# Performance work log

Hardware: AMD Instinct MI355X
Metric: run time of the kernel (lower is better)

Reference implementation:

```python
import jax, jax.numpy as jnp
import numpy as np

HIDDEN = 128
HEADS = 8
HEAD_DIM = HIDDEN // HEADS
N_NODES = 100000
N_EDGES = 1600000


def setup_inputs() -> dict:
    key = jax.random.key(0)
    ks = jax.random.split(key, 12)
    s = 1.0 / np.sqrt(HIDDEN)
    inp = {
        "x": jax.random.normal(ks[0], (N_NODES, HIDDEN), dtype=jnp.float32),
        "edge_index": jax.random.randint(ks[1], (2, N_EDGES), 0, N_NODES, dtype=jnp.int32),
        "edge_emb": jax.random.normal(ks[2], (N_EDGES, HIDDEN), dtype=jnp.float32),
        "q_w": jax.random.uniform(ks[3], (HIDDEN, HIDDEN), jnp.float32, -s, s),
        "q_b": jax.random.uniform(ks[4], (HIDDEN,), jnp.float32, -s, s),
        "k_w": jax.random.uniform(ks[5], (HIDDEN, HIDDEN), jnp.float32, -s, s),
        "k_b": jax.random.uniform(ks[6], (HIDDEN,), jnp.float32, -s, s),
        "v_w": jax.random.uniform(ks[7], (HIDDEN, HIDDEN), jnp.float32, -s, s),
        "v_b": jax.random.uniform(ks[8], (HIDDEN,), jnp.float32, -s, s),
        "out_w": jax.random.uniform(ks[9], (HIDDEN, HIDDEN), jnp.float32, -s, s),
        "out_b": jax.random.uniform(ks[10], (HIDDEN,), jnp.float32, -s, s),
        "eb_w": jax.random.uniform(ks[11], (HEADS, HIDDEN), jnp.float32, -s, s),
        "eb_b": jnp.zeros((HEADS,), dtype=jnp.float32),
    }
    return inp


def reference(x, edge_index, edge_emb, q_w, q_b, k_w, k_b, v_w, v_b, out_w, out_b, eb_w, eb_b):
    n = x.shape[0]
    # node projections -> [N, H, D]
    q = (x @ q_w.T + q_b).reshape(n, HEADS, HEAD_DIM)
    k = (x @ k_w.T + k_b).reshape(n, HEADS, HEAD_DIM)
    v = (x @ v_w.T + v_b).reshape(n, HEADS, HEAD_DIM)

    row, col = edge_index[0], edge_index[1]
    # per-edge scores: [E, H]
    scores = jnp.einsum('ehd,ehd->eh', q[row], k[col]) / jnp.sqrt(jnp.float32(HEAD_DIM))
    scores = scores + edge_emb @ eb_w.T + eb_b

    # segmented softmax over incoming edges of each destination node `row`
    seg_max = jax.ops.segment_max(scores, row, num_segments=n)  # [N, H]
    exp_scores = jnp.exp(scores - seg_max[row])
    seg_sum = jax.ops.segment_sum(exp_scores, row, num_segments=n)  # [N, H]
    attn = exp_scores / (seg_sum[row] + 1e-10)  # [E, H]

    # weighted scatter-aggregation of values
    weighted_v = attn[..., None] * v[col]  # [E, H, D]
    out = jax.ops.segment_sum(weighted_v, row, num_segments=n)  # [N, H, D]
    out = out.reshape(n, HIDDEN)
    return out @ out_w.T + out_b
```

## Files before the change

kernel.cpp:

```cpp
#include <hip/hip_runtime.h>

#define HID 128
#define NH 8

typedef __attribute__((ext_vector_type(8))) short short8;
typedef __attribute__((ext_vector_type(4))) float f32x4;
typedef __attribute__((ext_vector_type(2))) float f32x2;

__device__ __forceinline__ unsigned short f2bf(float f) {
    unsigned int u = __float_as_uint(f);
    u = (u + 0x7FFF + ((u >> 16) & 1)) >> 16;
    return (unsigned short)u;
}
__device__ __forceinline__ float bf2f(unsigned short s) {
    return __uint_as_float((unsigned int)s << 16);
}
__device__ __forceinline__ unsigned int pack2bf(float lo, float hi) {
    return (unsigned int)f2bf(lo) | ((unsigned int)f2bf(hi) << 16);
}

__global__ void k_init(const float* __restrict__ qw, const float* __restrict__ kw,
                       const float* __restrict__ vw, const float* __restrict__ ow,
                       unsigned short* __restrict__ wbf,
                       const int* __restrict__ row, int E, int* __restrict__ count) {
    int bid = blockIdx.x;
    int t = threadIdx.x;
    if (bid < 64) {
        int i = bid * 256 + t;
        int idx = i * 4;
        int m = idx >> 14;
        int off = idx & 16383;
        const float* src = (m == 0) ? qw : (m == 1) ? kw : (m == 2) ? vw : ow;
        float4 v = *(const float4*)(src + off);
        ushort4 o;
        o.x = f2bf(v.x); o.y = f2bf(v.y); o.z = f2bf(v.z); o.w = f2bf(v.w);
        *(ushort4*)(wbf + idx) = o;
    } else {
        int i = (bid - 64) * 256 + t;
        int stride = (gridDim.x - 64) * 256;
        for (; i < E; i += stride) atomicAdd(&count[row[i]], 1);
    }
}

__global__ void k_scan1(const int* __restrict__ in, int total,
                        int* __restrict__ out, int* __restrict__ bsums) {
    __shared__ int sd[256];
    int t = threadIdx.x;
    int base = blockIdx.x * 1024 + t * 4;
    int v0 = (base + 0 < total) ? in[base + 0] : 0;
    int v1 = (base + 1 < total) ? in[base + 1] : 0;
    int v2 = (base + 2 < total) ? in[base + 2] : 0;
    int v3 = (base + 3 < total) ? in[base + 3] : 0;
    int s = v0 + v1 + v2 + v3;
    sd[t] = s; __syncthreads();
    for (int off = 1; off < 256; off <<= 1) {
        int xx = (t >= off) ? sd[t - off] : 0;
        __syncthreads();
        sd[t] += xx;
        __syncthreads();
    }
    int excl = sd[t] - s;
    if (t == 255) bsums[blockIdx.x] = sd[255];
    int run = excl;
    if (base + 0 < total) out[base + 0] = run; run += v0;
    if (base + 1 < total) out[base + 1] = run; run += v1;
    if (base + 2 < total) out[base + 2] = run; run += v2;
    if (base + 3 < total) out[base + 3] = run;
}

__global__ void k_scan2(int* __restrict__ bs, int nb) {
    __shared__ int sd[128];
    int t = threadIdx.x;
    int vv = (t < nb) ? bs[t] : 0;
    sd[t] = vv; __syncthreads();
    for (int off = 1; off < 128; off <<= 1) {
        int xx = (t >= off) ? sd[t - off] : 0;
        __syncthreads();
        sd[t] += xx;
        __syncthreads();
    }
    if (t < nb) bs[t] = sd[t] - vv;
}

__global__ void k_scan3(int* __restrict__ out, int total, const int* __restrict__ bs) {
    int add = bs[blockIdx.x];
    int base = blockIdx.x * 1024 + threadIdx.x * 4;
    #pragma unroll
    for (int i = 0; i < 4; ++i)
        if (base + i < total) out[base + i] += add;
}

__global__ __launch_bounds__(256) void k_fat(
    const float* __restrict__ x, const unsigned short* __restrict__ wbf,
    const float* __restrict__ qb_, const float* __restrict__ kb_, const float* __restrict__ vb_,
    unsigned short* __restrict__ qkvbf, int n, int qblocks,
    const int* __restrict__ row, const int* __restrict__ col,
    const float* __restrict__ emb, const float* __restrict__ ebw,
    const float* __restrict__ ebb, const int* __restrict__ start,
    int* __restrict__ cursor, int* __restrict__ col_sorted,
    unsigned short* __restrict__ bias_s, int E)
{
    __shared__ __align__(16) char sm[17408];
    int bid = blockIdx.x;
    int t = threadIdx.x;

    if (bid < qblocks) {
        unsigned short (*xs)[136] = (unsigned short (*)[136])sm;
        int m0 = bid * 64;
        #pragma unroll
        for (int p = 0; p < 2; ++p) {
            int f = p * 256 + t;
            int r = f >> 3;
            int c16 = (f & 7) * 16;
            int node = m0 + r;
            float4 u0 = {0,0,0,0}, u1 = {0,0,0,0}, u2 = {0,0,0,0}, u3 = {0,0,0,0};
            if (node < n) {
                const float4* px = (const float4*)(x + (size_t)node * HID + c16);
                u0 = px[0]; u1 = px[1]; u2 = px[2]; u3 = px[3];
            }
            union { unsigned short u[8]; short8 v; } a, b;
            a.u[0]=f2bf(u0.x); a.u[1]=f2bf(u0.y); a.u[2]=f2bf(u0.z); a.u[3]=f2bf(u0.w);
            a.u[4]=f2bf(u1.x); a.u[5]=f2bf(u1.y); a.u[6]=f2bf(u1.z); a.u[7]=f2bf(u1.w);
            b.u[0]=f2bf(u2.x); b.u[1]=f2bf(u2.y); b.u[2]=f2bf(u2.z); b.u[3]=f2bf(u2.w);
            b.u[4]=f2bf(u3.x); b.u[5]=f2bf(u3.y); b.u[6]=f2bf(u3.z); b.u[7]=f2bf(u3.w);
            *(short8*)&xs[r][c16]     = a.v;
            *(short8*)&xs[r][c16 + 8] = b.v;
        }
        __syncthreads();

        int w = t >> 6, l = t & 63;
        int lr = l & 15, lc = l >> 4;
        short8 afr[4];
        #pragma unroll
        for (int c = 0; c < 4; ++c)
            afr[c] = *(const short8*)&xs[w * 16 + lr][c * 32 + lc * 8];

        #pragma unroll
        for (int m = 0; m < 3; ++m) {
            const float* bias = (m == 0) ? qb_ : (m == 1) ? kb_ : vb_;
            #pragma unroll
            for (int ct = 0; ct < 8; ++ct) {
                int colg = ct * 16 + lr;
                f32x4 acc = {0.f, 0.f, 0.f, 0.f};
                const unsigned short* wrow = wbf + (size_t)m * 16384 + (size_t)colg * 128 + lc * 8;
                #pragma unroll
                for (int c = 0; c < 4; ++c) {
                    short8 bfr = *(const short8*)(wrow + c * 32);
                    acc = __builtin_amdgcn_mfma_f32_16x16x32_bf16(afr[c], bfr, acc, 0, 0, 0);
                }
                float bv = bias[colg];
                #pragma unroll
                for (int r = 0; r < 4; ++r) {
                    int node = m0 + w * 16 + lc * 4 + r;
                    if (node < n)
                        qkvbf[(size_t)node * 384 + m * 128 + colg] = f2bf(acc[r] + bv);
                }
            }
        }
    } else {
        float (*Wx)[4][8][4] = (float (*)[4][8][4])sm;
        for (int i = t; i < 1024; i += 256) {
            int j = i & 3, g = (i >> 2) & 7, c = (i >> 5) & 3, h = i >> 7;
            Wx[h][c][g][j] = ebw[h * 128 + g * 16 + c * 4 + j];
        }
        float bbr[8];
        #pragma unroll
        for (int i = 0; i < 8; ++i) bbr[i] = ebb[i];
        __syncthreads();

        int l = t & 63;
        int g = l & 7;
        int sub = l >> 3;
        int e = (bid - qblocks) * 32 + (t >> 6) * 8 + sub;
        bool act = e < E;

        float p[8] = {0.f,0.f,0.f,0.f,0.f,0.f,0.f,0.f};
        if (act) {
            const float4* pe = (const float4*)(emb + (size_t)e * HID + g * 16);
            #pragma unroll
            for (int c = 0; c < 4; ++c) {
                float4 ev = pe[c];
                #pragma unroll
                for (int h = 0; h < 8; ++h) {
                    float4 wv = *(const float4*)&Wx[h][c][g][0];
                    p[h] += ev.x*wv.x + ev.y*wv.y + ev.z*wv.z + ev.w*wv.w;
                }
            }
        }
        #pragma unroll
        for (int off = 1; off < 8; off <<= 1) {
            #pragma unroll
            for (int h = 0; h < 8; ++h) p[h] += __shfl_xor(p[h], off);
        }
        if (act && g == 0) {
            int r = row[e];
            int ps = start[r] + atomicAdd(&cursor[r], 1);
            col_sorted[ps] = col[e];
            uint4 bv;
            bv.x = pack2bf(p[0] + bbr[0], p[1] + bbr[1]);
            bv.y = pack2bf(p[2] + bbr[2], p[3] + bbr[3]);
            bv.z = pack2bf(p[4] + bbr[4], p[5] + bbr[5]);
            bv.w = pack2bf(p[6] + bbr[6], p[7] + bbr[7]);
            *(uint4*)(bias_s + (size_t)ps * 8) = bv;
        }
    }
}

__global__ __launch_bounds__(256) void k_cvtk(
    const unsigned short* __restrict__ qkvbf, unsigned char* __restrict__ kp8, int n)
{
    int i = blockIdx.x * 256 + threadIdx.x;
    int node = i >> 4;
    int c8 = (i & 15) * 8;
    if (node >= n) return;
    short8 kv = *(const short8*)(qkvbf + (size_t)node * 384 + 128 + c8);
    float f[8];
    #pragma unroll
    for (int j = 0; j < 8; ++j) f[j] = bf2f((unsigned short)kv[j]);
    unsigned int lo = 0, hi = 0;
    lo = (unsigned int)__builtin_amdgcn_cvt_pk_fp8_f32(f[0], f[1], (int)lo, false);
    lo = (unsigned int)__builtin_amdgcn_cvt_pk_fp8_f32(f[2], f[3], (int)lo, true);
    hi = (unsigned int)__builtin_amdgcn_cvt_pk_fp8_f32(f[4], f[5], (int)hi, false);
    hi = (unsigned int)__builtin_amdgcn_cvt_pk_fp8_f32(f[6], f[7], (int)hi, true);
    uint2 o; o.x = lo; o.y = hi;
    *(uint2*)(kp8 + (size_t)node * HID + c8) = o;
}

__global__ __launch_bounds__(256) void k_attn(
    const unsigned short* __restrict__ qkvbf, const unsigned char* __restrict__ kp8,
    const int* __restrict__ cols, const unsigned short* __restrict__ bias_s,
    const int* __restrict__ start, unsigned short* __restrict__ aout, int n)
{
    int node = blockIdx.x * 4 + (threadIdx.x >> 6);
    if (node >= n) return;
    int l = threadIdx.x & 63;
    int slot = l >> 3;
    int h = l & 7;
    int s0 = start[node];
    int deg = start[node + 1] - s0;

    float qf[16];
    {
        const unsigned short* qp = qkvbf + (size_t)node * 384 + h * 16;
        short8 q0 = *(const short8*)qp;
        short8 q1 = *(const short8*)(qp + 8);
        #pragma unroll
        for (int i = 0; i < 8; ++i) {
            qf[i] = bf2f((unsigned short)q0[i]);
            qf[8 + i] = bf2f((unsigned short)q1[i]);
        }
    }

    float acc[16];
    #pragma unroll
    for (int i = 0; i < 16; ++i) acc[i] = 0.f;
    float denom = 0.f;

    for (int base = 0; base < deg; base += 8) {
        int idx = base + slot;
        bool act = idx < deg;
        int sidx = s0 + (act ? idx : 0);
        int c = act ? cols[sidx] : 0;
        float eb = act ? bf2f(bias_s[(size_t)sidx * 8 + h]) : 0.f;
        uint4 kw4 = *(const uint4*)(kp8 + (size_t)c * HID + h * 16);
        const unsigned short* vp = qkvbf + (size_t)c * 384 + 256 + h * 16;
        short8 va = *(const short8*)vp;
        short8 vb = *(const short8*)(vp + 8);

        float part = 0.f;
        {
            f32x2 d0 = __builtin_amdgcn_cvt_pk_f32_fp8((int)kw4.x, false);
            f32x2 d1 = __builtin_amdgcn_cvt_pk_f32_fp8((int)kw4.x, true);
            f32x2 d2 = __builtin_amdgcn_cvt_pk_f32_fp8((int)kw4.y, false);
            f32x2 d3 = __builtin_amdgcn_cvt_pk_f32_fp8((int)kw4.y, true);
            f32x2 d4 = __builtin_amdgcn_cvt_pk_f32_fp8((int)kw4.z, false);
            f32x2 d5 = __builtin_amdgcn_cvt_pk_f32_fp8((int)kw4.z, true);
            f32x2 d6 = __builtin_amdgcn_cvt_pk_f32_fp8((int)kw4.w, false);
            f32x2 d7 = __builtin_amdgcn_cvt_pk_f32_fp8((int)kw4.w, true);
            part += qf[0]*d0[0] + qf[1]*d0[1] + qf[2]*d1[0] + qf[3]*d1[1];
            part += qf[4]*d2[0] + qf[5]*d2[1] + qf[6]*d3[0] + qf[7]*d3[1];
            part += qf[8]*d4[0] + qf[9]*d4[1] + qf[10]*d5[0] + qf[11]*d5[1];
            part += qf[12]*d6[0] + qf[13]*d6[1] + qf[14]*d7[0] + qf[15]*d7[1];
        }
        float es = act ? __expf(part * 0.25f + eb) : 0.f;
        denom += es;
        #pragma unroll
        for (int i = 0; i < 8; ++i) acc[i]     += es * bf2f((unsigned short)va[i]);
        #pragma unroll
        for (int i = 0; i < 8; ++i) acc[8 + i] += es * bf2f((unsigned short)vb[i]);
    }

    #pragma unroll
    for (int off = 8; off < 64; off <<= 1) {
        denom += __shfl_xor(denom, off);
        #pragma unroll
        for (int i = 0; i < 16; ++i) acc[i] += __shfl_xor(acc[i], off);
    }
    if (slot == 0) {
        float inv = 1.f / (denom + 1e-10f);
        uint4 o0, o1;
        o0.x = pack2bf(acc[0]*inv,  acc[1]*inv);
        o0.y = pack2bf(acc[2]*inv,  acc[3]*inv);
        o0.z = pack2bf(acc[4]*inv,  acc[5]*inv);
        o0.w = pack2bf(acc[6]*inv,  acc[7]*inv);
        o1.x = pack2bf(acc[8]*inv,  acc[9]*inv);
        o1.y = pack2bf(acc[10]*inv, acc[11]*inv);
        o1.z = pack2bf(acc[12]*inv, acc[13]*inv);
        o1.w = pack2bf(acc[14]*inv, acc[15]*inv);
        unsigned short* op = aout + (size_t)node * HID + h * 16;
        *(uint4*)op       = o0;
        *(uint4*)(op + 8) = o1;
    }
}

__global__ __launch_bounds__(256) void k_outproj_mfma(
    const unsigned short* __restrict__ aout, const unsigned short* __restrict__ wbf,
    const float* __restrict__ ob, float* __restrict__ out, int n)
{
    __shared__ unsigned short hs[64][136];
    int t = threadIdx.x;
    int m0 = blockIdx.x * 64;
    #pragma unroll
    for (int p = 0; p < 4; ++p) {
        int f = p * 256 + t;
        int r = f >> 4;
        int c8 = (f & 15) * 8;
        int node = m0 + r;
        short8 val = {0,0,0,0,0,0,0,0};
        if (node < n) val = *(const short8*)(aout + (size_t)node * HID + c8);
        *(short8*)&hs[r][c8] = val;
    }
    __syncthreads();

    int w = t >> 6, l = t & 63;
    int lr = l & 15, lc = l >> 4;
    short8 afr[4];
    #pragma unroll
    for (int c = 0; c < 4; ++c)
        afr[c] = *(const short8*)&hs[w * 16 + lr][c * 32 + lc * 8];

    #pragma unroll
    for (int ct = 0; ct < 8; ++ct) {
        int colg = ct * 16 + lr;
        f32x4 acc = {0.f, 0.f, 0.f, 0.f};
        const unsigned short* wrow = wbf + (size_t)3 * 16384 + (size_t)colg * 128 + lc * 8;
        #pragma unroll
        for (int c = 0; c < 4; ++c) {
            short8 bfr = *(const short8*)(wrow + c * 32);
            acc = __builtin_amdgcn_mfma_f32_16x16x32_bf16(afr[c], bfr, acc, 0, 0, 0);
        }
        float bv = ob[colg];
        #pragma unroll
        for (int r = 0; r < 4; ++r) {
            int node = m0 + w * 16 + lc * 4 + r;
            if (node < n)
                out[(size_t)node * HID + colg] = acc[r] + bv;
        }
    }
}

extern "C" void kernel_launch(void* const* d_in, const int* in_sizes, int n_in,
                              void* d_out, int out_size, void* d_ws, size_t ws_size,
                              hipStream_t stream) {
    const float* x   = (const float*)d_in[0];
    const int*   eix = (const int*)  d_in[1];
    const float* emb = (const float*)d_in[2];
    const float* qw  = (const float*)d_in[3];
    const float* qb  = (const float*)d_in[4];
    const float* kw  = (const float*)d_in[5];
    const float* kb  = (const float*)d_in[6];
    const float* vw  = (const float*)d_in[7];
    const float* vb  = (const float*)d_in[8];
    const float* ow  = (const float*)d_in[9];
    const float* ob  = (const float*)d_in[10];
    const float* ebw = (const float*)d_in[11];
    const float* ebb = (const float*)d_in[12];

    int n = in_sizes[0] / HID;
    int E = in_sizes[2] / HID;
    const int* row = eix;
    const int* col = eix + E;

    char* wsp = (char*)d_ws;
    auto alloc = [&](size_t bytes) -> void* {
        void* p = (void*)wsp;
        wsp += (bytes + 255) & ~(size_t)255;
        return p;
    };
    unsigned short* qkvbf = (unsigned short*)alloc((size_t)n * 384 * 2);
    unsigned char* kp8    = (unsigned char*)alloc((size_t)n * HID);
    unsigned short* wbf   = (unsigned short*)alloc((size_t)4 * 16384 * 2);
    int* col_sorted       = (int*)alloc((size_t)E * 4);
    unsigned short* bias_s= (unsigned short*)alloc((size_t)E * 8 * 2);
    unsigned short* aout  = (unsigned short*)alloc((size_t)n * HID * 2);
    int* count            = (int*)alloc((size_t)(n + 2) * 4);
    int* startp           = (int*)alloc((size_t)(n + 2) * 4);
    int* bsums            = (int*)alloc(256 * 4);
    int* cursor           = (int*)alloc((size_t)n * 4);

    hipMemsetAsync(count, 0, (size_t)(n + 1) * sizeof(int), stream);
    hipMemsetAsync(cursor, 0, (size_t)n * sizeof(int), stream);

    k_init<<<64 + 2048, 256, 0, stream>>>(qw, kw, vw, ow, wbf, row, E, count);

    int total = n + 1;
    int nb = (total + 1023) / 1024;
    k_scan1<<<nb, 256, 0, stream>>>(count, total, startp, bsums);
    k_scan2<<<1, 128, 0, stream>>>(bsums, nb);
    k_scan3<<<nb, 256, 0, stream>>>(startp, total, bsums);

    int qblocks = (n + 63) / 64;
    int eblocks = (E + 31) / 32;
    k_fat<<<qblocks + eblocks, 256, 0, stream>>>(
        x, wbf, qb, kb, vb, qkvbf, n, qblocks,
        row, col, emb, ebw, ebb, startp, cursor, col_sorted, bias_s, E);

    k_cvtk<<<(n * 16 + 255) / 256, 256, 0, stream>>>(qkvbf, kp8, n);

    k_attn<<<(n + 3) / 4, 256, 0, stream>>>(qkvbf, kp8, col_sorted, bias_s,
                                            startp, aout, n);
    k_outproj_mfma<<<(n + 63) / 64, 256, 0, stream>>>(aout, wbf, ob, (float*)d_out, n);
}
```

Before: 557.2 us.

## Fold scan fixup into consumers, merge memsets, add L2 prewarm pass

Removes the k_scan3 fixup kernel: k_fat and k_attn now add the per-block prefix from bsums when they read start offsets. The two memsets become one by placing count and cursor next to each other in the workspace. It also adds a prewarm kernel that streams the qkv and fp8 key buffers just before attention so they sit in cache for the gathers. The prewarm costs a full extra read of about 100MB, and the scan change adds one extra load per lookup.

```diff
diff --git a/kernel.cpp b/kernel.cpp
--- a/kernel.cpp
+++ b/kernel.cpp
@@ -82,13 +82,6 @@
     if (t < nb) bs[t] = sd[t] - vv;
 }
 
-__global__ void k_scan3(int* __restrict__ out, int total, const int* __restrict__ bs) {
-    int add = bs[blockIdx.x];
-    int base = blockIdx.x * 1024 + threadIdx.x * 4;
-    #pragma unroll
-    for (int i = 0; i < 4; ++i)
-        if (base + i < total) out[base + i] += add;
-}
 
 __global__ __launch_bounds__(256) void k_fat(
     const float* __restrict__ x, const unsigned short* __restrict__ wbf,
@@ -96,9 +89,9 @@
     unsigned short* __restrict__ qkvbf, int n, int qblocks,
     const int* __restrict__ row, const int* __restrict__ col,
     const float* __restrict__ emb, const float* __restrict__ ebw,
-    const float* __restrict__ ebb, const int* __restrict__ start,
-    int* __restrict__ cursor, int* __restrict__ col_sorted,
-    unsigned short* __restrict__ bias_s, int E)
+    const float* __restrict__ ebb, const int* __restrict__ startp,
+    const int* __restrict__ bsums, int* __restrict__ cursor,
+    int* __restrict__ col_sorted, unsigned short* __restrict__ bias_s, int E)
 {
     __shared__ __align__(16) char sm[17408];
     int bid = blockIdx.x;
@@ -194,7 +187,8 @@
         }
         if (act && g == 0) {
             int r = row[e];
-            int ps = start[r] + atomicAdd(&cursor[r], 1);
+            int sg = startp[r] + bsums[r >> 10];
+            int ps = sg + atomicAdd(&cursor[r], 1);
             col_sorted[ps] = col[e];
             uint4 bv;
             bv.x = pack2bf(p[0] + bbr[0], p[1] + bbr[1]);
@@ -226,18 +220,33 @@
     *(uint2*)(kp8 + (size_t)node * HID + c8) = o;
 }
 
+__global__ __launch_bounds__(256) void k_prewarm(
+    const uint4* __restrict__ a, size_t n16, unsigned int* __restrict__ sink)
+{
+    size_t i = (size_t)blockIdx.x * 256 + threadIdx.x;
+    size_t stride = (size_t)gridDim.x * 256;
+    unsigned int s = 0;
+    for (; i < n16; i += stride) {
+        uint4 v = a[i];
+        s ^= v.x ^ v.y ^ v.z ^ v.w;
+    }
+    if (s == 0xDEADBEEFu) sink[blockIdx.x] = s;
+}
+
 __global__ __launch_bounds__(256) void k_attn(
     const unsigned short* __restrict__ qkvbf, const unsigned char* __restrict__ kp8,
     const int* __restrict__ cols, const unsigned short* __restrict__ bias_s,
-    const int* __restrict__ start, unsigned short* __restrict__ aout, int n)
+    const int* __restrict__ startp, const int* __restrict__ bsums,
+    unsigned short* __restrict__ aout, int n, int E)
 {
     int node = blockIdx.x * 4 + (threadIdx.x >> 6);
     if (node >= n) return;
     int l = threadIdx.x & 63;
     int slot = l >> 3;
     int h = l & 7;
-    int s0 = start[node];
-    int deg = start[node + 1] - s0;
+    int s0 = startp[node] + bsums[node >> 10];
+    int s1 = startp[node + 1] + bsums[(node + 1) >> 10];
+    int deg = s1 - s0;
 
     float qf[16];
     {
@@ -393,13 +402,15 @@
     int* col_sorted       = (int*)alloc((size_t)E * 4);
     unsigned short* bias_s= (unsigned short*)alloc((size_t)E * 8 * 2);
     unsigned short* aout  = (unsigned short*)alloc((size_t)n * HID * 2);
+    char* zbase           = (char*)alloc(0);
     int* count            = (int*)alloc((size_t)(n + 2) * 4);
+    int* cursor           = (int*)alloc((size_t)n * 4);
+    char* zend            = (char*)alloc(0);
     int* startp           = (int*)alloc((size_t)(n + 2) * 4);
     int* bsums            = (int*)alloc(256 * 4);
-    int* cursor           = (int*)alloc((size_t)n * 4);
-
-    hipMemsetAsync(count, 0, (size_t)(n + 1) * sizeof(int), stream);
-    hipMemsetAsync(cursor, 0, (size_t)n * sizeof(int), stream);
+    unsigned int* sink    = (unsigned int*)alloc(2048 * 4);
+
+    hipMemsetAsync(zbase, 0, (size_t)(zend - zbase), stream);
 
     k_init<<<64 + 2048, 256, 0, stream>>>(qw, kw, vw, ow, wbf, row, E, count);
 
@@ -407,17 +418,23 @@
     int nb = (total + 1023) / 1024;
     k_scan1<<<nb, 256, 0, stream>>>(count, total, startp, bsums);
     k_scan2<<<1, 128, 0, stream>>>(bsums, nb);
-    k_scan3<<<nb, 256, 0, stream>>>(startp, total, bsums);
 
     int qblocks = (n + 63) / 64;
     int eblocks = (E + 31) / 32;
     k_fat<<<qblocks + eblocks, 256, 0, stream>>>(
         x, wbf, qb, kb, vb, qkvbf, n, qblocks,
-        row, col, emb, ebw, ebb, startp, cursor, col_sorted, bias_s, E);
+        row, col, emb, ebw, ebb, startp, bsums, cursor, col_sorted, bias_s, E);
 
     k_cvtk<<<(n * 16 + 255) / 256, 256, 0, stream>>>(qkvbf, kp8, n);
 
+    {
+        char* beg = (char*)qkvbf;
+        char* end = (char*)kp8 + (size_t)n * HID;
+        size_t n16 = (size_t)(end - beg) / 16;
+        k_prewarm<<<2048, 256, 0, stream>>>((const uint4*)beg, n16, sink);
+    }
+
     k_attn<<<(n + 3) / 4, 256, 0, stream>>>(qkvbf, kp8, col_sorted, bias_s,
-                                            startp, aout, n);
+                                            startp, bsums, aout, n, E);
     k_outproj_mfma<<<(n + 63) / 64, 256, 0, stream>>>(aout, wbf, ob, (float*)d_out, n);
 }
```

Measured after the change: 561.1 us. About the same (+0.7%).
